# Kernel tuning notes

Hardware: AMD Instinct MI355X
Metric: run time of the kernel (lower is better)

## Reference

```python
import jax, jax.numpy as jnp
import numpy as np

EMBED = 1024
HEADS = 16
HEAD_SIZE = EMBED // HEADS


def setup_inputs() -> dict:
    key = jax.random.key(0)
    ks = jax.random.split(key, 12)
    B, S = 2, 2048
    s = 1.0 / np.sqrt(EMBED)
    return {
        "querys": jax.random.normal(ks[0], (B, S, EMBED), jnp.float32),
        "keys": jax.random.normal(ks[1], (B, S, EMBED), jnp.float32),
        "values": jax.random.normal(ks[2], (B, S, EMBED), jnp.float32),
        "Wq": jax.random.normal(ks[3], (EMBED, EMBED), jnp.float32) * s,
        "bq": jax.random.normal(ks[4], (EMBED,), jnp.float32) * s,
        "Wk": jax.random.normal(ks[5], (EMBED, EMBED), jnp.float32) * s,
        "bk": jax.random.normal(ks[6], (EMBED,), jnp.float32) * s,
        "Wv": jax.random.normal(ks[7], (EMBED, EMBED), jnp.float32) * s,
        "bv": jax.random.normal(ks[8], (EMBED,), jnp.float32) * s,
        "Wo": jax.random.normal(ks[9], (EMBED, EMBED), jnp.float32) * s,
        "bo": jax.random.normal(ks[10], (EMBED,), jnp.float32) * s,
    }


def reference(querys, keys, values, Wq, bq, Wk, bk, Wv, bv, Wo, bo):
    B, S, E = querys.shape
    H, D = HEADS, HEAD_SIZE
    # torch nn.Linear: y = x @ W.T + b
    q = (querys @ Wq.T + bq).reshape(B, S, H, D).transpose(0, 2, 1, 3)  # [B,H,S,D]
    k = (keys @ Wk.T + bk).reshape(B, S, H, D).transpose(0, 2, 1, 3)
    v = (values @ Wv.T + bv).reshape(B, S, H, D).transpose(0, 2, 1, 3)
    # NOTE: original scales by head_size**0.05 (faithful to source, likely a bug)
    scale = D ** 0.05
    energy = jnp.einsum("bhqd,bhkd->bhqk", q, k) / scale  # [B,H,S,S]
    attention = jax.nn.softmax(energy, axis=-1)
    out = jnp.einsum("bhqk,bhkd->bhqd", attention, v)  # [B,H,S,D]
    out = out.transpose(0, 2, 1, 3).reshape(B, S, E)
    return out @ Wo.T + bo
```

## Files before the change

kernel.cpp:

```cpp
#include <hip/hip_runtime.h>

typedef __attribute__((ext_vector_type(4))) float f32x4;
typedef __attribute__((ext_vector_type(8))) float f32x8;
typedef __attribute__((ext_vector_type(8))) unsigned short ushort8;
typedef __attribute__((ext_vector_type(4))) unsigned short ushort4v;
typedef __attribute__((ext_vector_type(8))) __bf16 bf16x8;

#define QSCALE 1.17183256f

#if __has_builtin(__builtin_amdgcn_exp2f)
#define EXP2(x) __builtin_amdgcn_exp2f(x)
#else
#define EXP2(x) exp2f(x)
#endif

__device__ __forceinline__ unsigned short f2bf(float x) {
  unsigned u = __float_as_uint(x);
  u += 0x7FFFu + ((u >> 16) & 1u);
  return (unsigned short)(u >> 16);
}

__device__ __forceinline__ ushort8 cvt8(const float* src) {
  float4 x0 = *(const float4*)src;
  float4 x1 = *(const float4*)(src + 4);
  ushort8 v;
  v[0] = f2bf(x0.x); v[1] = f2bf(x0.y); v[2] = f2bf(x0.z); v[3] = f2bf(x0.w);
  v[4] = f2bf(x1.x); v[5] = f2bf(x1.y); v[6] = f2bf(x1.z); v[7] = f2bf(x1.w);
  return v;
}

__device__ __forceinline__ f32x4 mfma16(ushort8 a, ushort8 b, f32x4 c) {
  return __builtin_amdgcn_mfma_f32_16x16x32_bf16(
      __builtin_bit_cast(bf16x8, a), __builtin_bit_cast(bf16x8, b), c, 0, 0, 0);
}
__device__ __forceinline__ f32x4 mfma16b(bf16x8 a, ushort8 b, f32x4 c) {
  return __builtin_amdgcn_mfma_f32_16x16x32_bf16(
      a, __builtin_bit_cast(bf16x8, b), c, 0, 0, 0);
}

__device__ __forceinline__ void gload_lds16(const void* g, void* l) {
  __builtin_amdgcn_global_load_lds(
      (const __attribute__((address_space(1))) void*)g,
      (__attribute__((address_space(3))) void*)l, 16, 0, 0);
}

__global__ __launch_bounds__(256) void cvt_f32_bf16(
    const float* __restrict__ s0, const float* __restrict__ s1, const float* __restrict__ s2,
    const float* __restrict__ s3, const float* __restrict__ s4, const float* __restrict__ s5,
    const float* __restrict__ s6, unsigned short* __restrict__ dstA,
    unsigned short* __restrict__ dstW)
{
  const int z = blockIdx.y;
  const float* src;
  unsigned short* dst;
  int n;
  if (z < 3) {
    src = (z == 0) ? s0 : (z == 1) ? s1 : s2;
    dst = dstA + (size_t)z * 4194304;
    n = 4194304;
  } else {
    src = (z == 3) ? s3 : (z == 4) ? s4 : (z == 5) ? s5 : s6;
    dst = dstW + (size_t)(z - 3) * 1048576;
    n = 1048576;
  }
  int i = (blockIdx.x * 256 + threadIdx.x) * 8;
  const int stride = gridDim.x * 256 * 8;
  for (; i < n; i += stride) *(ushort8*)(dst + i) = cvt8(src + i);
}

__global__ __launch_bounds__(256) void gemm_qkv_bf(
    const unsigned short* __restrict__ Abf, const unsigned short* __restrict__ Wbf,
    const float* __restrict__ bq, const float* __restrict__ bk, const float* __restrict__ bv,
    unsigned short* __restrict__ Qb, unsigned short* __restrict__ Kb,
    unsigned short* __restrict__ Vtb)
{
  __shared__ __align__(16) unsigned short Al[2][128 * 32];
  __shared__ __align__(16) unsigned short Wl[2][128 * 32];
  const int z = blockIdx.z;
  const unsigned short* Ap = Abf + (size_t)z * 4194304;
  const unsigned short* Wp = Wbf + (size_t)z * 1048576;
  const float* bp = (z == 0) ? bq : (z == 1) ? bk : bv;

  const int t = threadIdx.x, l = t & 63, w = t >> 6;
  const int lr = l & 15, g = l >> 4;
  const int wm = (w >> 1) * 64, wn = (w & 1) * 64;
  const int bx = blockIdx.x, by = blockIdx.y;

  int prow[2], pcol[2];
#pragma unroll
  for (int j = 0; j < 2; ++j) {
    int p = j * 256 + w * 64 + l;
    prow[j] = p >> 2;
    pcol[j] = (p & 3) ^ ((prow[j] >> 1) & 3);
  }

  f32x4 acc[4][4] = {};

#define STAGE_QKV(buf, k0)                                                        \
  {                                                                               \
    _Pragma("unroll") for (int j = 0; j < 2; ++j) {                               \
      gload_lds16(Ap + (size_t)(by * 128 + prow[j]) * 1024 + (k0) + pcol[j] * 8,  \
                  &Al[buf][(j * 256 + w * 64) * 8]);                              \
      gload_lds16(Wp + (size_t)(bx * 128 + prow[j]) * 1024 + (k0) + pcol[j] * 8,  \
                  &Wl[buf][(j * 256 + w * 64) * 8]);                              \
    }                                                                             \
  }

  STAGE_QKV(0, 0)
  __syncthreads();

  for (int kt = 0; kt < 32; ++kt) {
    const int cur = kt & 1;
    if (kt < 31) STAGE_QKV(cur ^ 1, (kt + 1) * 32)
    ushort8 a[4], b[4];
#pragma unroll
    for (int m = 0; m < 4; ++m) {
      int r = wm + m * 16 + lr;
      a[m] = *(const ushort8*)&Al[cur][r * 32 + (g ^ ((r >> 1) & 3)) * 8];
    }
#pragma unroll
    for (int n = 0; n < 4; ++n) {
      int r = wn + n * 16 + lr;
      b[n] = *(const ushort8*)&Wl[cur][r * 32 + (g ^ ((r >> 1) & 3)) * 8];
    }
#pragma unroll
    for (int m = 0; m < 4; ++m)
#pragma unroll
      for (int n = 0; n < 4; ++n)
        acc[m][n] = mfma16(a[m], b[n], acc[m][n]);
    __syncthreads();
  }

  float bias_n[4];
#pragma unroll
  for (int n = 0; n < 4; ++n) bias_n[n] = bp[bx * 128 + wn + n * 16 + lr];

  if (z < 2) {
    const float sc = (z == 0) ? QSCALE : 1.0f;
    unsigned short* Cp = z ? Kb : Qb;
#pragma unroll
    for (int m = 0; m < 4; ++m)
#pragma unroll
      for (int n = 0; n < 4; ++n)
#pragma unroll
        for (int r = 0; r < 4; ++r) {
          float v = (acc[m][n][r] + bias_n[n]) * sc;
          int gm = by * 128 + wm + m * 16 + g * 4 + r;
          int gn = bx * 128 + wn + n * 16 + lr;
          int bb = gm >> 11, s = gm & 2047;
          int h = gn >> 6, d = gn & 63;
          Cp[((size_t)((bb * 16 + h) * 2048 + s) << 6) + d] = f2bf(v);
        }
  } else {
#pragma unroll
    for (int m = 0; m < 4; ++m) {
      int gm0 = by * 128 + wm + m * 16 + g * 4;
      int bb = gm0 >> 11, s0 = gm0 & 2047;
#pragma unroll
      for (int n = 0; n < 4; ++n) {
        int gn = bx * 128 + wn + n * 16 + lr;
        int h = gn >> 6, d = gn & 63;
        ushort4v pk;
#pragma unroll
        for (int r = 0; r < 4; ++r) pk[r] = f2bf(acc[m][n][r] + bias_n[n]);
        *(ushort4v*)&Vtb[((size_t)((bb * 16 + h) * 64 + d) << 11) + s0] = pk;
      }
    }
  }
}

__global__ __launch_bounds__(256) void gemm_o_bf(
    const unsigned short* __restrict__ AO, const unsigned short* __restrict__ Wp,
    const float* __restrict__ bo, float* __restrict__ C)
{
  __shared__ __align__(16) unsigned short Al[2][128 * 32];
  __shared__ __align__(16) unsigned short Wl[2][64 * 32];
  const int t = threadIdx.x, l = t & 63, w = t >> 6;
  const int lr = l & 15, g = l >> 4;
  const int wm = w * 32;
  const int bx = blockIdx.x, by = blockIdx.y;

  int prow[2], pcol[2];
#pragma unroll
  for (int j = 0; j < 2; ++j) {
    int p = j * 256 + w * 64 + l;
    prow[j] = p >> 2;
    pcol[j] = (p & 3) ^ ((prow[j] >> 1) & 3);
  }

  f32x4 acc[2][4] = {};

#define STAGE_O(buf, k0)                                                          \
  {                                                                               \
    _Pragma("unroll") for (int j = 0; j < 2; ++j) {                               \
      gload_lds16(AO + (size_t)(by * 128 + prow[j]) * 1024 + (k0) + pcol[j] * 8,  \
                  &Al[buf][(j * 256 + w * 64) * 8]);                              \
    }                                                                             \
    gload_lds16(Wp + (size_t)(bx * 64 + prow[0]) * 1024 + (k0) + pcol[0] * 8,     \
                &Wl[buf][(w * 64) * 8]);                                          \
  }

  STAGE_O(0, 0)
  __syncthreads();

  for (int kt = 0; kt < 32; ++kt) {
    const int cur = kt & 1;
    if (kt < 31) STAGE_O(cur ^ 1, (kt + 1) * 32)
    ushort8 a[2], b[4];
#pragma unroll
    for (int m = 0; m < 2; ++m) {
      int r = wm + m * 16 + lr;
      a[m] = *(const ushort8*)&Al[cur][r * 32 + (g ^ ((r >> 1) & 3)) * 8];
    }
#pragma unroll
    for (int n = 0; n < 4; ++n) {
      int r = n * 16 + lr;
      b[n] = *(const ushort8*)&Wl[cur][r * 32 + (g ^ ((r >> 1) & 3)) * 8];
    }
#pragma unroll
    for (int m = 0; m < 2; ++m)
#pragma unroll
      for (int n = 0; n < 4; ++n)
        acc[m][n] = mfma16(a[m], b[n], acc[m][n]);
    __syncthreads();
  }

  float bias_n[4];
#pragma unroll
  for (int n = 0; n < 4; ++n) bias_n[n] = bo[bx * 64 + n * 16 + lr];

#pragma unroll
  for (int m = 0; m < 2; ++m)
#pragma unroll
    for (int n = 0; n < 4; ++n)
#pragma unroll
      for (int r = 0; r < 4; ++r) {
        int gm = by * 128 + wm + m * 16 + g * 4 + r;
        int gn = bx * 64 + n * 16 + lr;
        C[(size_t)gm * 1024 + gn] = acc[m][n][r] + bias_n[n];
      }
}

__global__ __launch_bounds__(256) void attn_fwd(
    const unsigned short* __restrict__ Qb, const unsigned short* __restrict__ Kb,
    const unsigned short* __restrict__ Vtb, unsigned short* __restrict__ AO)
{
  __shared__ __align__(16) unsigned short Kl[2][64 * 64];
  __shared__ __align__(16) unsigned short Vl[2][64 * 64];
  const int t = threadIdx.x;
  const int l = t & 63, w = t >> 6;
  const int lr = l & 15, g = l >> 4;
  const int qt = blockIdx.x, bh = blockIdx.y;
  const unsigned short* Qh = Qb + (size_t)bh * (2048 * 64);
  const unsigned short* Kh = Kb + (size_t)bh * (2048 * 64);
  const unsigned short* Vth = Vtb + (size_t)bh * (64 * 2048);

  ushort8 aq[2][2];
#pragma unroll
  for (int m = 0; m < 2; ++m)
#pragma unroll
    for (int kk = 0; kk < 2; ++kk) {
      int q = qt * 128 + w * 32 + m * 16 + lr;
      aq[m][kk] = *(const ushort8*)&Qh[q * 64 + kk * 32 + g * 8];
    }

  f32x4 o[2][4] = {};
  float lsp[2] = {0.f, 0.f};

  const int sr = t >> 2, sc4 = t & 3;
  ushort8 rk[2], rv[2];

#pragma unroll
  for (int i = 0; i < 2; ++i) {
    rk[i] = *(const ushort8*)&Kh[(0 * 64 + sr) * 64 + (sc4 + i * 4) * 8];
    rv[i] = *(const ushort8*)&Vth[sr * 2048 + 0 * 64 + (sc4 + i * 4) * 8];
  }
#pragma unroll
  for (int i = 0; i < 2; ++i) {
    int c = sc4 + i * 4;
    *(ushort8*)&Kl[0][sr * 64 + ((c ^ (sr & 7))) * 8] = rk[i];
#pragma unroll
    for (int h = 0; h < 2; ++h) {
      int tw = 2 * c + h;
      int n = tw >> 2, gg = tw & 3;
      int chunk = ((n >> 1) << 2) + gg;
      int within = (n & 1) << 2;
      ushort4v hv = h ? __builtin_shufflevector(rv[i], rv[i], 4, 5, 6, 7)
                      : __builtin_shufflevector(rv[i], rv[i], 0, 1, 2, 3);
      *(ushort4v*)&Vl[0][sr * 64 + ((chunk ^ (sr & 7))) * 8 + within] = hv;
    }
  }
  __syncthreads();

  for (int kt = 0; kt < 32; ++kt) {
    const int cur = kt & 1;
    if (kt < 31) {
#pragma unroll
      for (int i = 0; i < 2; ++i) {
        rk[i] = *(const ushort8*)&Kh[((kt + 1) * 64 + sr) * 64 + (sc4 + i * 4) * 8];
        rv[i] = *(const ushort8*)&Vth[sr * 2048 + (kt + 1) * 64 + (sc4 + i * 4) * 8];
      }
    }

    f32x4 s[4][2] = {};
#pragma unroll
    for (int kk = 0; kk < 2; ++kk) {
      ushort8 ak[4];
#pragma unroll
      for (int n = 0; n < 4; ++n)
        ak[n] = *(const ushort8*)&Kl[cur][(n * 16 + lr) * 64 + (((kk * 4 + g) ^ (lr & 7))) * 8];
      __builtin_amdgcn_s_setprio(1);
#pragma unroll
      for (int n = 0; n < 4; ++n)
#pragma unroll
        for (int m = 0; m < 2; ++m)
          s[n][m] = mfma16(ak[n], aq[m][kk], s[n][m]);
      __builtin_amdgcn_s_setprio(0);
    }

    bf16x8 pa[2][2];
#pragma unroll
    for (int m = 0; m < 2; ++m) {
      float p[4][4];
      float sum = 0.f;
#pragma unroll
      for (int n = 0; n < 4; ++n)
#pragma unroll
        for (int r = 0; r < 4; ++r) {
          p[n][r] = EXP2(s[n][m][r]);
          sum += p[n][r];
        }
      lsp[m] += sum;
      f32x8 v0 = {p[0][0], p[0][1], p[0][2], p[0][3], p[1][0], p[1][1], p[1][2], p[1][3]};
      f32x8 v1 = {p[2][0], p[2][1], p[2][2], p[2][3], p[3][0], p[3][1], p[3][2], p[3][3]};
      pa[m][0] = __builtin_convertvector(v0, bf16x8);
      pa[m][1] = __builtin_convertvector(v1, bf16x8);
    }

#pragma unroll
    for (int kk = 0; kk < 2; ++kk) {
#pragma unroll
      for (int n = 0; n < 4; ++n) {
        int d = n * 16 + lr;
        ushort8 bv = *(const ushort8*)&Vl[cur][d * 64 + (((kk * 4 + g) ^ (lr & 7))) * 8];
        __builtin_amdgcn_s_setprio(1);
#pragma unroll
        for (int m = 0; m < 2; ++m)
          o[m][n] = mfma16b(pa[m][kk], bv, o[m][n]);
        __builtin_amdgcn_s_setprio(0);
      }
    }

    if (kt < 31) {
      const int nb = cur ^ 1;
#pragma unroll
      for (int i = 0; i < 2; ++i) {
        int c = sc4 + i * 4;
        *(ushort8*)&Kl[nb][sr * 64 + ((c ^ (sr & 7))) * 8] = rk[i];
#pragma unroll
        for (int h = 0; h < 2; ++h) {
          int tw = 2 * c + h;
          int n = tw >> 2, gg = tw & 3;
          int chunk = ((n >> 1) << 2) + gg;
          int within = (n & 1) << 2;
          ushort4v hv = h ? __builtin_shufflevector(rv[i], rv[i], 4, 5, 6, 7)
                          : __builtin_shufflevector(rv[i], rv[i], 0, 1, 2, 3);
          *(ushort4v*)&Vl[nb][sr * 64 + ((chunk ^ (sr & 7))) * 8 + within] = hv;
        }
      }
    }
    __syncthreads();
  }

  const int bb = bh >> 4, h = bh & 15;
#pragma unroll
  for (int m = 0; m < 2; ++m) {
    float v = lsp[m];
    v += __shfl_xor(v, 16);
    v += __shfl_xor(v, 32);
    float iv = 1.0f / v;
    float ivr[4];
#pragma unroll
    for (int r = 0; r < 4; ++r) ivr[r] = __shfl(iv, (l >> 4) * 20 + r);
#pragma unroll
    for (int n = 0; n < 4; ++n)
#pragma unroll
      for (int r = 0; r < 4; ++r) {
        int q = qt * 128 + w * 32 + m * 16 + g * 4 + r;
        AO[(size_t)(bb * 2048 + q) * 1024 + h * 64 + n * 16 + lr] =
            f2bf(o[m][n][r] * ivr[r]);
      }
  }
}

__global__ __launch_bounds__(256) void gemm_qkv_f32(
    const float* __restrict__ Aq, const float* __restrict__ Ak, const float* __restrict__ Av,
    const float* __restrict__ Wq, const float* __restrict__ Wk, const float* __restrict__ Wv,
    const float* __restrict__ bq, const float* __restrict__ bk, const float* __restrict__ bv,
    unsigned short* __restrict__ Qb, unsigned short* __restrict__ Kb, unsigned short* __restrict__ Vtb)
{
  __shared__ __align__(16) unsigned short Al[128 * 32];
  __shared__ __align__(16) unsigned short Wl[128 * 32];
  const int z = blockIdx.z;
  const float* Ap = (z == 0) ? Aq : (z == 1) ? Ak : Av;
  const float* Wp = (z == 0) ? Wq : (z == 1) ? Wk : Wv;
  const float* bp = (z == 0) ? bq : (z == 1) ? bk : bv;

  const int t = threadIdx.x;
  const int l = t & 63, w = t >> 6;
  const int lr = l & 15, g = l >> 4;
  const int wm = (w >> 1) * 64, wn = (w & 1) * 64;
  const int bx = blockIdx.x, by = blockIdx.y;
  const int r0 = t >> 2, c0 = t & 3;

  f32x4 acc[4][4] = {};

  for (int k0 = 0; k0 < 1024; k0 += 32) {
    __syncthreads();
#pragma unroll
    for (int i = 0; i < 2; ++i) {
      int r = r0 + i * 64;
      int cs = c0 ^ ((r >> 1) & 3);
      *(ushort8*)&Al[r * 32 + cs * 8] = cvt8(Ap + (size_t)(by * 128 + r) * 1024 + k0 + c0 * 8);
      *(ushort8*)&Wl[r * 32 + cs * 8] = cvt8(Wp + (size_t)(bx * 128 + r) * 1024 + k0 + c0 * 8);
    }
    __syncthreads();
    ushort8 a[4], b[4];
#pragma unroll
    for (int m = 0; m < 4; ++m) {
      int r = wm + m * 16 + lr;
      a[m] = *(const ushort8*)&Al[r * 32 + (g ^ ((r >> 1) & 3)) * 8];
    }
#pragma unroll
    for (int n = 0; n < 4; ++n) {
      int r = wn + n * 16 + lr;
      b[n] = *(const ushort8*)&Wl[r * 32 + (g ^ ((r >> 1) & 3)) * 8];
    }
#pragma unroll
    for (int m = 0; m < 4; ++m)
#pragma unroll
      for (int n = 0; n < 4; ++n)
        acc[m][n] = mfma16(a[m], b[n], acc[m][n]);
  }

  float bias_n[4];
#pragma unroll
  for (int n = 0; n < 4; ++n) bias_n[n] = bp[bx * 128 + wn + n * 16 + lr];

  if (z < 2) {
    const float sc = (z == 0) ? QSCALE : 1.0f;
    unsigned short* Cp = z ? Kb : Qb;
#pragma unroll
    for (int m = 0; m < 4; ++m)
#pragma unroll
      for (int n = 0; n < 4; ++n)
#pragma unroll
        for (int r = 0; r < 4; ++r) {
          float v = (acc[m][n][r] + bias_n[n]) * sc;
          int gm = by * 128 + wm + m * 16 + g * 4 + r;
          int gn = bx * 128 + wn + n * 16 + lr;
          int bb = gm >> 11, s = gm & 2047;
          int h = gn >> 6, d = gn & 63;
          Cp[((size_t)((bb * 16 + h) * 2048 + s) << 6) + d] = f2bf(v);
        }
  } else {
#pragma unroll
    for (int m = 0; m < 4; ++m) {
      int gm0 = by * 128 + wm + m * 16 + g * 4;
      int bb = gm0 >> 11, s0 = gm0 & 2047;
#pragma unroll
      for (int n = 0; n < 4; ++n) {
        int gn = bx * 128 + wn + n * 16 + lr;
        int h = gn >> 6, d = gn & 63;
        ushort4v pk;
#pragma unroll
        for (int r = 0; r < 4; ++r) pk[r] = f2bf(acc[m][n][r] + bias_n[n]);
        *(ushort4v*)&Vtb[((size_t)((bb * 16 + h) * 64 + d) << 11) + s0] = pk;
      }
    }
  }
}

__global__ __launch_bounds__(256) void gemm_o_f32(
    const unsigned short* __restrict__ AO, const float* __restrict__ Wo,
    const float* __restrict__ bo, float* __restrict__ C)
{
  __shared__ __align__(16) unsigned short Al[128 * 32];
  __shared__ __align__(16) unsigned short Wl[64 * 32];
  const int t = threadIdx.x;
  const int l = t & 63, w = t >> 6;
  const int lr = l & 15, g = l >> 4;
  const int wm = w * 32;
  const int bx = blockIdx.x, by = blockIdx.y;
  const int r0 = t >> 2, c0 = t & 3;

  f32x4 acc[2][4] = {};

  for (int k0 = 0; k0 < 1024; k0 += 32) {
    __syncthreads();
#pragma unroll
    for (int i = 0; i < 2; ++i) {
      int r = r0 + i * 64;
      int cs = c0 ^ ((r >> 1) & 3);
      *(ushort8*)&Al[r * 32 + cs * 8] =
          *(const ushort8*)&AO[(size_t)(by * 128 + r) * 1024 + k0 + c0 * 8];
    }
    {
      int r = r0;
      int cs = c0 ^ ((r >> 1) & 3);
      *(ushort8*)&Wl[r * 32 + cs * 8] = cvt8(Wo + (size_t)(bx * 64 + r) * 1024 + k0 + c0 * 8);
    }
    __syncthreads();
    ushort8 a[2], b[4];
#pragma unroll
    for (int m = 0; m < 2; ++m) {
      int r = wm + m * 16 + lr;
      a[m] = *(const ushort8*)&Al[r * 32 + (g ^ ((r >> 1) & 3)) * 8];
    }
#pragma unroll
    for (int n = 0; n < 4; ++n) {
      int r = n * 16 + lr;
      b[n] = *(const ushort8*)&Wl[r * 32 + (g ^ ((r >> 1) & 3)) * 8];
    }
#pragma unroll
    for (int m = 0; m < 2; ++m)
#pragma unroll
      for (int n = 0; n < 4; ++n)
        acc[m][n] = mfma16(a[m], b[n], acc[m][n]);
  }

  float bias_n[4];
#pragma unroll
  for (int n = 0; n < 4; ++n) bias_n[n] = bo[bx * 64 + n * 16 + lr];

#pragma unroll
  for (int m = 0; m < 2; ++m)
#pragma unroll
    for (int n = 0; n < 4; ++n)
#pragma unroll
      for (int r = 0; r < 4; ++r) {
        int gm = by * 128 + wm + m * 16 + g * 4 + r;
        int gn = bx * 64 + n * 16 + lr;
        C[(size_t)gm * 1024 + gn] = acc[m][n][r] + bias_n[n];
      }
}

extern "C" void kernel_launch(void* const* d_in, const int* in_sizes, int n_in,
                              void* d_out, int out_size, void* d_ws, size_t ws_size,
                              hipStream_t stream) {
  (void)in_sizes; (void)n_in; (void)out_size;
  const float* querys = (const float*)d_in[0];
  const float* keys   = (const float*)d_in[1];
  const float* values = (const float*)d_in[2];
  const float* Wq = (const float*)d_in[3];
  const float* bq = (const float*)d_in[4];
  const float* Wk = (const float*)d_in[5];
  const float* bk = (const float*)d_in[6];
  const float* Wv = (const float*)d_in[7];
  const float* bv = (const float*)d_in[8];
  const float* Wo = (const float*)d_in[9];
  const float* bo = (const float*)d_in[10];

  const size_t need = (size_t)29360128 * 2;
  if (ws_size >= need) {
    unsigned short* Wbf = (unsigned short*)d_ws;
    unsigned short* Qb  = Wbf + 4194304;
    unsigned short* Kb  = Qb + 4194304;
    unsigned short* Vtb = Kb + 4194304;
    unsigned short* Abf = Vtb + 4194304;
    unsigned short* AO  = Abf;

    cvt_f32_bf16<<<dim3(1024, 7), 256, 0, stream>>>(querys, keys, values, Wq, Wk, Wv, Wo,
                                                    Abf, Wbf);
    gemm_qkv_bf<<<dim3(8, 32, 3), 256, 0, stream>>>(Abf, Wbf, bq, bk, bv, Qb, Kb, Vtb);
    attn_fwd<<<dim3(16, 32), 256, 0, stream>>>(Qb, Kb, Vtb, AO);
    gemm_o_bf<<<dim3(16, 32), 256, 0, stream>>>(AO, Wbf + 3 * 1048576, bo, (float*)d_out);
  } else {
    unsigned short* Qb  = (unsigned short*)d_ws;
    unsigned short* Kb  = Qb + (size_t)4194304;
    unsigned short* Vtb = Kb + (size_t)4194304;
    unsigned short* AO  = Vtb + (size_t)4194304;

    gemm_qkv_f32<<<dim3(8, 32, 3), 256, 0, stream>>>(querys, keys, values, Wq, Wk, Wv,
                                                     bq, bk, bv, Qb, Kb, Vtb);
    attn_fwd<<<dim3(16, 32), 256, 0, stream>>>(Qb, Kb, Vtb, AO);
    gemm_o_f32<<<dim3(16, 32), 256, 0, stream>>>(AO, Wo, bo, (float*)d_out);
  }
}
```

Before: 138.7 us.

## Use 8 waves per attention block and compute softmax row sums via MFMA

The attention kernel now launches 512 threads per block, so each wave handles 16 query rows instead of 32. Register pressure per wave drops and more waves are available to hide latency. Each thread stages one K/V chunk instead of two. The softmax denominators are accumulated with an extra MFMA against a vector of ones instead of scalar sums plus cross-lane shuffles. This removes the reduction and shuffle work at the end, at the cost of one more MFMA per k-step and less reuse of each K/V LDS read across query rows. The V-read swizzle now uses d&7 rather than lr&7, which is the same value since d = n*16+lr.

New measurement: 136.4 us. No clear change (-1.6%).

```diff
diff --git a/kernel.cpp b/kernel.cpp
--- a/kernel.cpp
+++ b/kernel.cpp
@@ -241,7 +241,7 @@
       }
 }
 
-__global__ __launch_bounds__(256) void attn_fwd(
+__global__ __launch_bounds__(512) void attn_fwd(
     const unsigned short* __restrict__ Qb, const unsigned short* __restrict__ Kb,
     const unsigned short* __restrict__ Vtb, unsigned short* __restrict__ AO)
 {
@@ -255,142 +255,102 @@
   const unsigned short* Kh = Kb + (size_t)bh * (2048 * 64);
   const unsigned short* Vth = Vtb + (size_t)bh * (64 * 2048);
 
-  ushort8 aq[2][2];
-#pragma unroll
-  for (int m = 0; m < 2; ++m)
-#pragma unroll
-    for (int kk = 0; kk < 2; ++kk) {
-      int q = qt * 128 + w * 32 + m * 16 + lr;
-      aq[m][kk] = *(const ushort8*)&Qh[q * 64 + kk * 32 + g * 8];
-    }
-
-  f32x4 o[2][4] = {};
-  float lsp[2] = {0.f, 0.f};
-
-  const int sr = t >> 2, sc4 = t & 3;
-  ushort8 rk[2], rv[2];
-
-#pragma unroll
-  for (int i = 0; i < 2; ++i) {
-    rk[i] = *(const ushort8*)&Kh[(0 * 64 + sr) * 64 + (sc4 + i * 4) * 8];
-    rv[i] = *(const ushort8*)&Vth[sr * 2048 + 0 * 64 + (sc4 + i * 4) * 8];
-  }
-#pragma unroll
-  for (int i = 0; i < 2; ++i) {
-    int c = sc4 + i * 4;
-    *(ushort8*)&Kl[0][sr * 64 + ((c ^ (sr & 7))) * 8] = rk[i];
-#pragma unroll
-    for (int h = 0; h < 2; ++h) {
-      int tw = 2 * c + h;
-      int n = tw >> 2, gg = tw & 3;
-      int chunk = ((n >> 1) << 2) + gg;
-      int within = (n & 1) << 2;
-      ushort4v hv = h ? __builtin_shufflevector(rv[i], rv[i], 4, 5, 6, 7)
-                      : __builtin_shufflevector(rv[i], rv[i], 0, 1, 2, 3);
-      *(ushort4v*)&Vl[0][sr * 64 + ((chunk ^ (sr & 7))) * 8 + within] = hv;
-    }
-  }
+  ushort8 aq[2];
+#pragma unroll
+  for (int kk = 0; kk < 2; ++kk) {
+    int q = qt * 128 + w * 16 + lr;
+    aq[kk] = *(const ushort8*)&Qh[q * 64 + kk * 32 + g * 8];
+  }
+
+  ushort8 ones;
+#pragma unroll
+  for (int j = 0; j < 8; ++j) ones[j] = 0x3F80;
+
+  f32x4 o[4] = {};
+  f32x4 lacc = {};
+
+  const int sr = t >> 3, sc = t & 7;
+  ushort8 rk, rv;
+
+#define STAGE_ATTN(buf)                                                      \
+  {                                                                          \
+    *(ushort8*)&Kl[buf][sr * 64 + ((sc ^ (sr & 7))) * 8] = rk;               \
+    _Pragma("unroll") for (int h = 0; h < 2; ++h) {                          \
+      int tw = 2 * sc + h;                                                   \
+      int n4 = tw >> 2, gg = tw & 3;                                         \
+      int chunk = ((n4 >> 1) << 2) + gg;                                     \
+      int within = (n4 & 1) << 2;                                            \
+      ushort4v hv = h ? __builtin_shufflevector(rv, rv, 4, 5, 6, 7)          \
+                      : __builtin_shufflevector(rv, rv, 0, 1, 2, 3);         \
+      *(ushort4v*)&Vl[buf][sr * 64 + ((chunk ^ (sr & 7))) * 8 + within] = hv;\
+    }                                                                        \
+  }
+
+  rk = *(const ushort8*)&Kh[sr * 64 + sc * 8];
+  rv = *(const ushort8*)&Vth[sr * 2048 + sc * 8];
+  STAGE_ATTN(0)
   __syncthreads();
 
   for (int kt = 0; kt < 32; ++kt) {
     const int cur = kt & 1;
     if (kt < 31) {
-#pragma unroll
-      for (int i = 0; i < 2; ++i) {
-        rk[i] = *(const ushort8*)&Kh[((kt + 1) * 64 + sr) * 64 + (sc4 + i * 4) * 8];
-        rv[i] = *(const ushort8*)&Vth[sr * 2048 + (kt + 1) * 64 + (sc4 + i * 4) * 8];
+      rk = *(const ushort8*)&Kh[((kt + 1) * 64 + sr) * 64 + sc * 8];
+      rv = *(const ushort8*)&Vth[sr * 2048 + (kt + 1) * 64 + sc * 8];
+    }
+
+    f32x4 s[4] = {};
+    __builtin_amdgcn_s_setprio(1);
+#pragma unroll
+    for (int kk = 0; kk < 2; ++kk) {
+#pragma unroll
+      for (int n = 0; n < 4; ++n) {
+        ushort8 ak = *(const ushort8*)&Kl[cur][(n * 16 + lr) * 64 +
+                                              (((kk * 4 + g) ^ (lr & 7))) * 8];
+        s[n] = mfma16(ak, aq[kk], s[n]);
       }
     }
-
-    f32x4 s[4][2] = {};
+    __builtin_amdgcn_s_setprio(0);
+
+    float p[4][4];
+#pragma unroll
+    for (int n = 0; n < 4; ++n)
+#pragma unroll
+      for (int r = 0; r < 4; ++r) p[n][r] = EXP2(s[n][r]);
+    f32x8 v0 = {p[0][0], p[0][1], p[0][2], p[0][3], p[1][0], p[1][1], p[1][2], p[1][3]};
+    f32x8 v1 = {p[2][0], p[2][1], p[2][2], p[2][3], p[3][0], p[3][1], p[3][2], p[3][3]};
+    bf16x8 pa[2];
+    pa[0] = __builtin_convertvector(v0, bf16x8);
+    pa[1] = __builtin_convertvector(v1, bf16x8);
+
+    __builtin_amdgcn_s_setprio(1);
 #pragma unroll
     for (int kk = 0; kk < 2; ++kk) {
-      ushort8 ak[4];
-#pragma unroll
-      for (int n = 0; n < 4; ++n)
-        ak[n] = *(const ushort8*)&Kl[cur][(n * 16 + lr) * 64 + (((kk * 4 + g) ^ (lr & 7))) * 8];
-      __builtin_amdgcn_s_setprio(1);
-#pragma unroll
-      for (int n = 0; n < 4; ++n)
-#pragma unroll
-        for (int m = 0; m < 2; ++m)
-          s[n][m] = mfma16(ak[n], aq[m][kk], s[n][m]);
-      __builtin_amdgcn_s_setprio(0);
-    }
-
-    bf16x8 pa[2][2];
-#pragma unroll
-    for (int m = 0; m < 2; ++m) {
-      float p[4][4];
-      float sum = 0.f;
-#pragma unroll
-      for (int n = 0; n < 4; ++n)
-#pragma unroll
-        for (int r = 0; r < 4; ++r) {
-          p[n][r] = EXP2(s[n][m][r]);
-          sum += p[n][r];
-        }
-      lsp[m] += sum;
-      f32x8 v0 = {p[0][0], p[0][1], p[0][2], p[0][3], p[1][0], p[1][1], p[1][2], p[1][3]};
-      f32x8 v1 = {p[2][0], p[2][1], p[2][2], p[2][3], p[3][0], p[3][1], p[3][2], p[3][3]};
-      pa[m][0] = __builtin_convertvector(v0, bf16x8);
-      pa[m][1] = __builtin_convertvector(v1, bf16x8);
-    }
-
-#pragma unroll
-    for (int kk = 0; kk < 2; ++kk) {
+      lacc = mfma16b(pa[kk], ones, lacc);
 #pragma unroll
       for (int n = 0; n < 4; ++n) {
         int d = n * 16 + lr;
-        ushort8 bv = *(const ushort8*)&Vl[cur][d * 64 + (((kk * 4 + g) ^ (lr & 7))) * 8];
-        __builtin_amdgcn_s_setprio(1);
-#pragma unroll
-        for (int m = 0; m < 2; ++m)
-          o[m][n] = mfma16b(pa[m][kk], bv, o[m][n]);
-        __builtin_amdgcn_s_setprio(0);
+        ushort8 bv = *(const ushort8*)&Vl[cur][d * 64 + (((kk * 4 + g) ^ (d & 7))) * 8];
+        o[n] = mfma16b(pa[kk], bv, o[n]);
       }
     }
-
-    if (kt < 31) {
-      const int nb = cur ^ 1;
-#pragma unroll
-      for (int i = 0; i < 2; ++i) {
-        int c = sc4 + i * 4;
-        *(ushort8*)&Kl[nb][sr * 64 + ((c ^ (sr & 7))) * 8] = rk[i];
-#pragma unroll
-        for (int h = 0; h < 2; ++h) {
-          int tw = 2 * c + h;
-          int n = tw >> 2, gg = tw & 3;
-          int chunk = ((n >> 1) << 2) + gg;
-          int within = (n & 1) << 2;
-          ushort4v hv = h ? __builtin_shufflevector(rv[i], rv[i], 4, 5, 6, 7)
-                          : __builtin_shufflevector(rv[i], rv[i], 0, 1, 2, 3);
-          *(ushort4v*)&Vl[nb][sr * 64 + ((chunk ^ (sr & 7))) * 8 + within] = hv;
-        }
-      }
-    }
+    __builtin_amdgcn_s_setprio(0);
+
+    if (kt < 31) STAGE_ATTN(cur ^ 1)
     __syncthreads();
   }
 
   const int bb = bh >> 4, h = bh & 15;
-#pragma unroll
-  for (int m = 0; m < 2; ++m) {
-    float v = lsp[m];
-    v += __shfl_xor(v, 16);
-    v += __shfl_xor(v, 32);
-    float iv = 1.0f / v;
-    float ivr[4];
-#pragma unroll
-    for (int r = 0; r < 4; ++r) ivr[r] = __shfl(iv, (l >> 4) * 20 + r);
-#pragma unroll
-    for (int n = 0; n < 4; ++n)
-#pragma unroll
-      for (int r = 0; r < 4; ++r) {
-        int q = qt * 128 + w * 32 + m * 16 + g * 4 + r;
-        AO[(size_t)(bb * 2048 + q) * 1024 + h * 64 + n * 16 + lr] =
-            f2bf(o[m][n][r] * ivr[r]);
-      }
-  }
+  float inv[4];
+#pragma unroll
+  for (int r = 0; r < 4; ++r) inv[r] = 1.0f / lacc[r];
+#pragma unroll
+  for (int n = 0; n < 4; ++n)
+#pragma unroll
+    for (int r = 0; r < 4; ++r) {
+      int q = qt * 128 + w * 16 + g * 4 + r;
+      AO[(size_t)(bb * 2048 + q) * 1024 + h * 64 + n * 16 + lr] =
+          f2bf(o[n][r] * inv[r]);
+    }
 }
 
 __global__ __launch_bounds__(256) void gemm_qkv_f32(
@@ -573,7 +533,7 @@
     cvt_f32_bf16<<<dim3(1024, 7), 256, 0, stream>>>(querys, keys, values, Wq, Wk, Wv, Wo,
                                                     Abf, Wbf);
     gemm_qkv_bf<<<dim3(8, 32, 3), 256, 0, stream>>>(Abf, Wbf, bq, bk, bv, Qb, Kb, Vtb);
-    attn_fwd<<<dim3(16, 32), 256, 0, stream>>>(Qb, Kb, Vtb, AO);
+    attn_fwd<<<dim3(16, 32), 512, 0, stream>>>(Qb, Kb, Vtb, AO);
     gemm_o_bf<<<dim3(16, 32), 256, 0, stream>>>(AO, Wbf + 3 * 1048576, bo, (float*)d_out);
   } else {
     unsigned short* Qb  = (unsigned short*)d_ws;
@@ -583,7 +543,7 @@
 
     gemm_qkv_f32<<<dim3(8, 32, 3), 256, 0, stream>>>(querys, keys, values, Wq, Wk, Wv,
                                                      bq, bk, bv, Qb, Kb, Vtb);
-    attn_fwd<<<dim3(16, 32), 256, 0, stream>>>(Qb, Kb, Vtb, AO);
+    attn_fwd<<<dim3(16, 32), 512, 0, stream>>>(Qb, Kb, Vtb, AO);
     gemm_o_f32<<<dim3(16, 32), 256, 0, stream>>>(AO, Wo, bo, (float*)d_out);
   }
 }
```
